# Kernel tuning notes

Measured on AMD Instinct MI355X. Metric: run time of the kernel, lower is better.

The kernel has to match this reference:

```python
import jax, jax.numpy as jnp
import numpy as np

N, E = 50000, 1600000
IN, HID, OUT, H, ED = 128, 16, 40, 4, 16
HC = HID * H  # 64
NEG_SLOPE = 0.2
EPS = 1e-16


def gat_conv(x, src, dst, e_attr, W, att_s, att_d, We, att_e, bias):
    # x: [N, Fin]; src/dst: [E_tot]; e_attr: [E_tot, ED]
    n = x.shape[0]
    h = (x @ W).reshape(n, H, HID)                      # [N,H,C]
    a_s = (h * att_s).sum(-1)                           # [N,H]
    a_d = (h * att_d).sum(-1)                           # [N,H]
    ee = (e_attr @ We).reshape(-1, H, HID)              # [E,H,C]
    a_e = (ee * att_e).sum(-1)                          # [E,H]
    alpha = a_s[src] + a_d[dst] + a_e                   # [E,H]
    alpha = jax.nn.leaky_relu(alpha, NEG_SLOPE)
    amax = jax.ops.segment_max(alpha, dst, num_segments=n)
    ex = jnp.exp(alpha - amax[dst])
    den = jax.ops.segment_sum(ex, dst, num_segments=n)
    alpha = ex / (den[dst] + EPS)
    msg = h[src] * alpha[..., None]                     # [E,H,C]
    out = jax.ops.segment_sum(msg, dst, num_segments=n) # [N,H,C]
    return out.reshape(n, HC) + bias


def setup_inputs() -> dict:
    key = jax.random.key(0)
    ks = jax.random.split(key, 20)
    s = 0.05
    inp = {
        "x": jax.random.normal(ks[0], (N, IN), jnp.float32),
        "edge_index": jax.random.randint(ks[1], (2, E), 0, N, jnp.int64 if jax.config.jax_enable_x64 else jnp.int32),
        "edge_attr": jax.random.normal(ks[2], (E, ED), jnp.float32),
        # conv1
        "W1": jax.random.normal(ks[3], (IN, HC)) * s,
        "att_src1": jax.random.normal(ks[4], (H, HID)) * s,
        "att_dst1": jax.random.normal(ks[5], (H, HID)) * s,
        "We1": jax.random.normal(ks[6], (ED, HC)) * s,
        "att_e1": jax.random.normal(ks[7], (H, HID)) * s,
        "b1": jnp.zeros((HC,), jnp.float32),
        # conv2
        "W2": jax.random.normal(ks[8], (HC, HC)) * s,
        "att_src2": jax.random.normal(ks[9], (H, HID)) * s,
        "att_dst2": jax.random.normal(ks[10], (H, HID)) * s,
        "We2": jax.random.normal(ks[11], (ED, HC)) * s,
        "att_e2": jax.random.normal(ks[12], (H, HID)) * s,
        "b2": jnp.zeros((HC,), jnp.float32),
        # head
        "lw1": jax.random.normal(ks[13], (HC, HID)) * s,
        "lb1": jnp.zeros((HID,), jnp.float32),
        "lw2": jax.random.normal(ks[14], (HID, OUT)) * s,
        "lb2": jnp.zeros((OUT,), jnp.float32),
    }
    return inp


def reference(x, edge_index, edge_attr,
              W1, att_src1, att_dst1, We1, att_e1, b1,
              W2, att_src2, att_dst2, We2, att_e2, b2,
              lw1, lb1, lw2, lb2):
    n = x.shape[0]
    loop = jnp.arange(n, dtype=edge_index.dtype)
    src = jnp.concatenate([edge_index[0], loop])
    dst = jnp.concatenate([edge_index[1], loop])
    # self-loop edge_attr filled with mean over edges (PyG fill_value='mean')
    mean_attr = edge_attr.mean(axis=0, keepdims=True)
    ea = jnp.concatenate([edge_attr, jnp.broadcast_to(mean_attr, (n, edge_attr.shape[1]))])

    h = gat_conv(x, src, dst, ea, W1, att_src1, att_dst1, We1, att_e1, b1)
    h = jax.nn.relu(h)  # dropout is identity at eval
    h = gat_conv(h, src, dst, ea, W2, att_src2, att_dst2, We2, att_e2, b2)
    h = jax.nn.relu(h)
    h = (h @ lw1 + lb1) @ lw2 + lb2  # Linear -> Dropout(eval) -> Linear
    return jax.nn.log_softmax(h, axis=1)
```

## Files before the change

kernel.cpp:

```cpp
#include <hip/hip_runtime.h>
#include <hip/hip_fp16.h>

#define N_NODES 50000
#define E_EDGES 1600000
#define NEG 0.2f
#define EDGE_BLOCKS 6250
#define RED_BLOCKS 64
#define SCAN_BLOCKS ((N_NODES + 255)/256)

__device__ __forceinline__ float lrelu(float x){ return fmaxf(x, NEG*x); }
__device__ __forceinline__ float bcastlane(float v, int k){
    return __int_as_float(__builtin_amdgcn_readlane(__float_as_int(v), k));
}
__device__ __forceinline__ unsigned bf16rn(float x){
    unsigned u = __float_as_uint(x);
    return (u + 0x7FFFu + ((u >> 16) & 1u)) >> 16;
}
__device__ __forceinline__ float bf2f(unsigned short u){
    return __uint_as_float(((unsigned)u) << 16);
}
__device__ __forceinline__ unsigned h16(float x){
    return (unsigned)__half_as_ushort(__float2half(x));
}
__device__ __forceinline__ float f16dec(unsigned u){
    return __half2float(__ushort_as_half((unsigned short)(u & 0xFFFFu)));
}

#if __has_builtin(__builtin_amdgcn_cvt_f32_fp8) && __has_builtin(__builtin_amdgcn_cvt_pk_fp8_f32)
__device__ __forceinline__ unsigned enc8(float x){
    return (unsigned)__builtin_amdgcn_cvt_pk_fp8_f32(x, x, 0, false) & 0xFFu;
}
__device__ __forceinline__ float dec8(unsigned b){
    return __builtin_amdgcn_cvt_f32_fp8((int)b, 0);
}
#else
__device__ __forceinline__ unsigned enc8(float x){
    float ax = fabsf(x); unsigned s = (x < 0.f) ? 0x80u : 0u;
    if (ax < 0.015625f){
        int q = (int)rintf(ax * 512.f);
        return s | (unsigned)q;
    }
    if (ax >= 448.f) return s | 0x7Eu;
    int ee; float mm = frexpf(ax, &ee);
    int q = (int)rintf(mm * 16.f);
    int E = ee + 6;
    if (q == 16){ q = 8; ++E; }
    if (E > 15){ return s | 0x7Eu; }
    return s | ((unsigned)E << 3) | (unsigned)(q - 8);
}
__device__ __forceinline__ float dec8(unsigned b){
    unsigned s = b >> 7, e = (b >> 3) & 15u, m = b & 7u;
    float mag = e ? __uint_as_float(((e + 120u) << 23) | (m << 20))
                  : (float)m * 0.001953125f;
    return s ? -mag : mag;
}
#endif


__global__ void k_prep1(const float* __restrict__ We1, const float* __restrict__ atte1,
                        const float* __restrict__ We2, const float* __restrict__ atte2,
                        float* __restrict__ small){
    int t = threadIdx.x;
    int k = t >> 2, hh = t & 3;
    float w1 = 0.f, w2 = 0.f;
    for (int c = 0; c < 16; ++c){
        w1 = fmaf(We1[k*64 + hh*16 + c], atte1[hh*16 + c], w1);
        w2 = fmaf(We2[k*64 + hh*16 + c], atte2[hh*16 + c], w2);
    }
    small[32 + t] = w1;
    small[96 + t] = w2;
}

__global__ __launch_bounds__(256) void k_hist(const int4* __restrict__ dst4, int* __restrict__ deg,
                                              ushort4* __restrict__ rank4){
    int i = blockIdx.x*256 + threadIdx.x;
    if (i < E_EDGES/4){
        int4 v = dst4[i];
        ushort4 r;
        r.x = (unsigned short)atomicAdd(&deg[v.x], 1);
        r.y = (unsigned short)atomicAdd(&deg[v.y], 1);
        r.z = (unsigned short)atomicAdd(&deg[v.z], 1);
        r.w = (unsigned short)atomicAdd(&deg[v.w], 1);
        rank4[i] = r;
    }
}

__global__ __launch_bounds__(256) void k_scan_a(const int* __restrict__ deg, int* __restrict__ bsum){
    int i = blockIdx.x*256 + threadIdx.x;
    int v = (i < N_NODES) ? deg[i] : 0;
    v += __shfl_xor(v,1); v += __shfl_xor(v,2); v += __shfl_xor(v,4);
    v += __shfl_xor(v,8); v += __shfl_xor(v,16); v += __shfl_xor(v,32);
    __shared__ int ws[4];
    if ((threadIdx.x & 63) == 0) ws[threadIdx.x >> 6] = v;
    __syncthreads();
    if (threadIdx.x == 0) bsum[blockIdx.x] = ws[0] + ws[1] + ws[2] + ws[3];
}

__global__ __launch_bounds__(256) void k_scan_b(const int* __restrict__ bsum, int* __restrict__ boff){
    __shared__ int sm[256];
    int t = threadIdx.x;
    int v = (t < SCAN_BLOCKS) ? bsum[t] : 0;
    sm[t] = v;
    __syncthreads();
    for (int off = 1; off < 256; off <<= 1){
        int u = (t >= off) ? sm[t-off] : 0;
        __syncthreads();
        sm[t] += u;
        __syncthreads();
    }
    boff[t] = (t > 0) ? sm[t-1] : 0;
    if (t == 0) boff[SCAN_BLOCKS] = sm[255];
}

__global__ __launch_bounds__(256) void k_scan_c(const int* __restrict__ deg, const int* __restrict__ boff,
                                                int* __restrict__ base){
    int i = blockIdx.x*256 + threadIdx.x;
    int lane = threadIdx.x & 63, wid = threadIdx.x >> 6;
    int v = (i < N_NODES) ? deg[i] : 0;
    int inc = v;
    for (int off = 1; off < 64; off <<= 1){
        int u = __shfl_up(inc, off);
        if (lane >= off) inc += u;
    }
    __shared__ int wsum[4];
    if (lane == 63) wsum[wid] = inc;
    __syncthreads();
    int wpre = 0;
#pragma unroll
    for (int w = 0; w < 4; ++w) wpre += (w < wid) ? wsum[w] : 0;
    int ex = boff[blockIdx.x] + wpre + inc - v;
    if (i < N_NODES) base[i] = ex;
    if (i == N_NODES - 1) base[N_NODES] = ex + v;
}

template<int FIN>
__global__ __launch_bounds__(256) void k_node(const float* __restrict__ in, const float* __restrict__ W,
                                              const float* __restrict__ att_s, const float* __restrict__ att_d,
                                              unsigned char* __restrict__ hb8,
                                              unsigned short* __restrict__ a_s,
                                              unsigned short* __restrict__ a_d){
    __shared__ float Wl[FIN*64];
    for (int i = threadIdx.x; i < FIN*64; i += 256) Wl[i] = W[i];
    __syncthreads();
    int lane = threadIdx.x & 63;
    int node = blockIdx.x*4 + (threadIdx.x >> 6);
    const float* row = in + (size_t)node*FIN;
    float x0 = row[lane];
    float x1 = 0.f;
    if constexpr (FIN == 128) x1 = row[64 + lane];
    float acc = 0.f;
#pragma unroll
    for (int k = 0; k < 64; ++k)
        acc = fmaf(bcastlane(x0, k), Wl[k*64 + lane], acc);
    if constexpr (FIN == 128){
#pragma unroll
        for (int k = 0; k < 64; ++k)
            acc = fmaf(bcastlane(x1, k), Wl[(64+k)*64 + lane], acc);
    }
    hb8[(size_t)node*64 + lane] = (unsigned char)enc8(acc);
    float ps = acc * att_s[lane];
    float pd = acc * att_d[lane];
    ps += __shfl_xor(ps,1); ps += __shfl_xor(ps,2); ps += __shfl_xor(ps,4); ps += __shfl_xor(ps,8);
    pd += __shfl_xor(pd,1); pd += __shfl_xor(pd,2); pd += __shfl_xor(pd,4); pd += __shfl_xor(pd,8);
    if ((lane & 15) == 0){
        a_s[node*4 + (lane>>4)] = (unsigned short)bf16rn(ps);
        a_d[node*4 + (lane>>4)] = (unsigned short)bf16rn(pd);
    }
}

__global__ __launch_bounds__(256) void k_edges(const int* __restrict__ src, const int* __restrict__ dst,
                                               const unsigned short* __restrict__ rank,
                                               const float* __restrict__ ea, const float* __restrict__ small,
                                               const int* __restrict__ base, uint4* __restrict__ rec,
                                               float* __restrict__ partials){
    __shared__ float w1[64], w2[64];
    __shared__ float red[64];
    if (threadIdx.x < 64){ w1[threadIdx.x] = small[32+threadIdx.x]; w2[threadIdx.x] = small[96+threadIdx.x]; }
    __syncthreads();
    int e = blockIdx.x*256 + threadIdx.x;
    int s = src[e], d = dst[e];
    int rk = (int)rank[e];
    int p = base[d] + rk;
    const float4* eap = (const float4*)(ea + (size_t)e*16);
    float cs[16];
    float ae1[4] = {0,0,0,0}, ae2[4] = {0,0,0,0};
#pragma unroll
    for (int q = 0; q < 4; ++q){
        float4 v4 = eap[q];
        float vv[4] = {v4.x, v4.y, v4.z, v4.w};
#pragma unroll
        for (int r = 0; r < 4; ++r){
            int k = q*4 + r;
            float xv = vv[r];
            cs[k] = xv;
#pragma unroll
            for (int hh = 0; hh < 4; ++hh){
                ae1[hh] = fmaf(xv, w1[k*4+hh], ae1[hh]);
                ae2[hh] = fmaf(xv, w2[k*4+hh], ae2[hh]);
            }
        }
    }
    unsigned q8[4];
#pragma unroll
    for (int hh = 0; hh < 4; ++hh){
        int qv = (int)rintf(ae2[hh]*256.f) + 128;
        qv = qv < 0 ? 0 : (qv > 255 ? 255 : qv);
        q8[hh] = (unsigned)qv;
    }
    uint4 r;
    r.x = (unsigned)s;
    r.y = h16(ae1[0]) | (h16(ae1[1]) << 16);
    r.z = h16(ae1[2]) | (h16(ae1[3]) << 16);
    r.w = q8[0] | (q8[1] << 8) | (q8[2] << 16) | (q8[3] << 24);
    rec[p] = r;
#pragma unroll
    for (int k = 0; k < 16; ++k){
        float v = cs[k];
        v += __shfl_xor(v,1); v += __shfl_xor(v,2); v += __shfl_xor(v,4);
        v += __shfl_xor(v,8); v += __shfl_xor(v,16); v += __shfl_xor(v,32);
        if ((threadIdx.x & 63) == 0) red[k*4 + (threadIdx.x>>6)] = v;
    }
    __syncthreads();
    if (threadIdx.x < 16){
        float v = red[threadIdx.x*4] + red[threadIdx.x*4+1] + red[threadIdx.x*4+2] + red[threadIdx.x*4+3];
        partials[blockIdx.x*16 + threadIdx.x] = v;
    }
}

__global__ __launch_bounds__(256) void k_red(const float* __restrict__ partials, float* __restrict__ red16){
    const int TOT = EDGE_BLOCKS*16;
    int t = threadIdx.x;
    float v = 0.f;
    for (int idx = blockIdx.x*256 + t; idx < TOT; idx += RED_BLOCKS*256) v += partials[idx];
    v += __shfl_xor(v,16); v += __shfl_xor(v,32);
    __shared__ float sm[64];
    int lane = t & 63, wid = t >> 6;
    if (lane < 16) sm[wid*16 + lane] = v;
    __syncthreads();
    if (t < 16) red16[blockIdx.x*16 + t] = sm[t] + sm[16+t] + sm[32+t] + sm[48+t];
}

__global__ __launch_bounds__(256) void k_prep2(float* __restrict__ small, const float* __restrict__ red16){
    __shared__ float sm[256];
    __shared__ float mean_s[16];
    int t = threadIdx.x;
    float v = 0.f;
    for (int r = (t>>4); r < RED_BLOCKS; r += 16) v += red16[r*16 + (t&15)];
    sm[t] = v;
    __syncthreads();
    if (t < 16){
        float s = 0.f;
#pragma unroll
        for (int i = 0; i < 16; ++i) s += sm[t + 16*i];
        float m = s * (1.0f/(float)E_EDGES);
        mean_s[t] = m; small[16+t] = m;
    }
    __syncthreads();
    if (t < 4){
        float a1 = 0.f, a2 = 0.f;
#pragma unroll
        for (int k = 0; k < 16; ++k){
            a1 = fmaf(mean_s[k], small[32 + k*4 + t], a1);
            a2 = fmaf(mean_s[k], small[96 + k*4 + t], a2);
        }
        small[160+t] = a1; small[164+t] = a2;
    }
}

template<int L>
__global__ __launch_bounds__(256) void k_agg(const uint4* __restrict__ recs, const int* __restrict__ base,
                                             const unsigned char* __restrict__ hb8,
                                             const unsigned short* __restrict__ a_s,
                                             const unsigned short* __restrict__ a_d,
                                             const float* __restrict__ aeloop, const float* __restrict__ bias,
                                             float* __restrict__ out){
    int lane = threadIdx.x & 63;
    int n = blockIdx.x*4 + (threadIdx.x >> 6);
    int hh = lane >> 4;
    int e16 = lane >> 2, h4 = lane & 3;
    float ad_acc = bf2f(a_d[n*4+hh]);
    float ad_w   = bf2f(a_d[n*4+h4]);
    float wL = __expf(lrelu(bf2f(a_s[n*4+hh]) + ad_acc + aeloop[hh]));
    float s0 = wL, s1 = 0.f;
    float acc0 = wL * dec8(hb8[(unsigned)n*64u + (unsigned)lane]);
    float acc1 = 0.f;
    int b0 = base[n], b1 = base[n+1];
    for (int pc = b0; pc < b1; pc += 16){
        int m = b1 - pc; m = m < 16 ? m : 16;
        float w = 0.f;
        unsigned si_e = 0u;
        if (e16 < m){
            uint4 r = recs[pc + e16];
            si_e = r.x;
            float ae;
            if constexpr (L == 1){
                ae = f16dec(((h4 < 2) ? r.y : r.z) >> ((h4 & 1)*16));
            } else {
                ae = (float)((int)((r.w >> (h4*8)) & 255u) - 128) * 0.00390625f;
            }
            float as_v = bf2f((unsigned short)a_s[si_e*4u + (unsigned)h4]);
            w = __expf(lrelu(as_v + ad_w + ae));
        }
        int j = 0;
        for (; j + 2 <= m; j += 2){
            unsigned siA = (unsigned)__shfl((int)si_e, j*4);
            unsigned siB = (unsigned)__shfl((int)si_e, j*4 + 4);
            float wA = __shfl(w, j*4 + hh);
            float wB = __shfl(w, j*4 + 4 + hh);
            float hvA = dec8(hb8[siA*64u + (unsigned)lane]);
            float hvB = dec8(hb8[siB*64u + (unsigned)lane]);
            s0 += wA; acc0 = fmaf(wA, hvA, acc0);
            s1 += wB; acc1 = fmaf(wB, hvB, acc1);
        }
        if (j < m){
            unsigned si = (unsigned)__shfl((int)si_e, j*4);
            float wj = __shfl(w, j*4 + hh);
            float hv = dec8(hb8[si*64u + (unsigned)lane]);
            s0 += wj; acc0 = fmaf(wj, hv, acc0);
        }
    }
    float s = s0 + s1;
    float val = (acc0 + acc1) / (s + 1e-16f) + bias[lane];
    out[(size_t)n*64 + lane] = fmaxf(val, 0.f);
}

__global__ __launch_bounds__(256) void k_head(const float* __restrict__ h2,
                                              const float* __restrict__ lw1, const float* __restrict__ lb1,
                                              const float* __restrict__ lw2, const float* __restrict__ lb2,
                                              float* __restrict__ out){
    int n = blockIdx.x*256 + threadIdx.x;
    if (n >= N_NODES) return;
    float y16[16];
#pragma unroll
    for (int j = 0; j < 16; ++j) y16[j] = lb1[j];
    const float4* hp = (const float4*)(h2 + (size_t)n*64);
#pragma unroll
    for (int k4 = 0; k4 < 16; ++k4){
        float4 hv = hp[k4];
        float hvv[4] = {hv.x, hv.y, hv.z, hv.w};
#pragma unroll
        for (int r = 0; r < 4; ++r){
            float x = hvv[r];
            int k = k4*4 + r;
#pragma unroll
            for (int j = 0; j < 16; ++j) y16[j] = fmaf(x, lw1[k*16+j], y16[j]);
        }
    }
    float y[40];
#pragma unroll
    for (int o = 0; o < 40; ++o) y[o] = lb2[o];
#pragma unroll
    for (int j = 0; j < 16; ++j){
        float x = y16[j];
#pragma unroll
        for (int o = 0; o < 40; ++o) y[o] = fmaf(x, lw2[j*40+o], y[o]);
    }
    float mx = y[0];
#pragma unroll
    for (int o = 1; o < 40; ++o) mx = fmaxf(mx, y[o]);
    float sum = 0.f;
#pragma unroll
    for (int o = 0; o < 40; ++o) sum += __expf(y[o] - mx);
    float ls = __logf(sum) + mx;
    float* op = out + (size_t)n*40;
#pragma unroll
    for (int o = 0; o < 40; ++o) op[o] = y[o] - ls;
}

extern "C" void kernel_launch(void* const* d_in, const int* in_sizes, int n_in,
                              void* d_out, int out_size, void* d_ws, size_t ws_size,
                              hipStream_t stream){
    const float* x     = (const float*)d_in[0];
    const int*   ei    = (const int*)  d_in[1];
    const float* ea    = (const float*)d_in[2];
    const float* W1    = (const float*)d_in[3];
    const float* atts1 = (const float*)d_in[4];
    const float* attd1 = (const float*)d_in[5];
    const float* We1   = (const float*)d_in[6];
    const float* atte1 = (const float*)d_in[7];
    const float* b1    = (const float*)d_in[8];
    const float* W2    = (const float*)d_in[9];
    const float* atts2 = (const float*)d_in[10];
    const float* attd2 = (const float*)d_in[11];
    const float* We2   = (const float*)d_in[12];
    const float* atte2 = (const float*)d_in[13];
    const float* b2    = (const float*)d_in[14];
    const float* lw1   = (const float*)d_in[15];
    const float* lb1   = (const float*)d_in[16];
    const float* lw2   = (const float*)d_in[17];
    const float* lb2   = (const float*)d_in[18];
    float* outp = (float*)d_out;

    const int* srcp = ei;
    const int* dstp = ei + E_EDGES;

    char* ws = (char*)d_ws;
    size_t off = 0;
    auto alloc = [&](size_t bytes) -> void* {
        void* p = ws + off;
        off = (off + bytes + 255) & ~(size_t)255;
        return p;
    };
    float*  smallf   = (float*) alloc(256*sizeof(float));
    float*  partials = (float*) alloc((size_t)EDGE_BLOCKS*16*sizeof(float));
    float*  red16    = (float*) alloc((size_t)RED_BLOCKS*16*sizeof(float));
    int*    deg      = (int*)   alloc((size_t)N_NODES*sizeof(int));
    int*    base     = (int*)   alloc((size_t)(N_NODES+1)*sizeof(int));
    int*    bsum     = (int*)   alloc((size_t)(SCAN_BLOCKS+1)*sizeof(int));
    int*    boff     = (int*)   alloc((size_t)(SCAN_BLOCKS+1)*sizeof(int));
    unsigned short* rank = (unsigned short*)alloc((size_t)E_EDGES*sizeof(unsigned short));
    uint4*  rec      = (uint4*) alloc((size_t)E_EDGES*16);
    unsigned char* hb8 = (unsigned char*)alloc((size_t)N_NODES*64);
    float*  obuf     = (float*) alloc((size_t)N_NODES*64*sizeof(float));
    unsigned short* asb = (unsigned short*)alloc((size_t)N_NODES*4*sizeof(unsigned short));
    unsigned short* adb = (unsigned short*)alloc((size_t)N_NODES*4*sizeof(unsigned short));

    const int NB = N_NODES/4;
    const int HB = (N_NODES + 255)/256;

    hipMemsetAsync(deg, 0, (size_t)N_NODES*sizeof(int), stream);
    k_prep1<<<1, 64, 0, stream>>>(We1, atte1, We2, atte2, smallf);
    k_hist<<<(E_EDGES/4 + 255)/256, 256, 0, stream>>>((const int4*)dstp, deg, (ushort4*)rank);
    k_scan_a<<<SCAN_BLOCKS, 256, 0, stream>>>(deg, bsum);
    k_scan_b<<<1, 256, 0, stream>>>(bsum, boff);
    k_scan_c<<<SCAN_BLOCKS, 256, 0, stream>>>(deg, boff, base);

    k_node<128><<<NB, 256, 0, stream>>>(x, W1, atts1, attd1, hb8, asb, adb);
    k_edges<<<EDGE_BLOCKS, 256, 0, stream>>>(srcp, dstp, rank, ea, smallf, base, rec, partials);
    k_red<<<RED_BLOCKS, 256, 0, stream>>>(partials, red16);
    k_prep2<<<1, 256, 0, stream>>>(smallf, red16);
    k_agg<1><<<NB, 256, 0, stream>>>(rec, base, hb8, asb, adb, smallf + 160, b1, obuf);

    k_node<64><<<NB, 256, 0, stream>>>(obuf, W2, atts2, attd2, hb8, asb, adb);
    k_agg<2><<<NB, 256, 0, stream>>>(rec, base, hb8, asb, adb, smallf + 164, b2, obuf);

    k_head<<<HB, 256, 0, stream>>>(obuf, lw1, lb1, lw2, lb2, outp);
}
```

Before: 348.6 us.

## Replace global atomic degree histogram with per-block LDS histograms plus column scan

```diff
diff --git a/kernel.cpp b/kernel.cpp
--- a/kernel.cpp
+++ b/kernel.cpp
@@ -7,6 +7,9 @@
 #define EDGE_BLOCKS 6250
 #define RED_BLOCKS 64
 #define SCAN_BLOCKS ((N_NODES + 255)/256)
+#define HBLK 128
+#define EPHB (E_EDGES/HBLK)
+#define NPAIR (N_NODES/2)
 
 __device__ __forceinline__ float lrelu(float x){ return fmaxf(x, NEG*x); }
 __device__ __forceinline__ float bcastlane(float v, int k){
@@ -71,18 +74,39 @@
     small[96 + t] = w2;
 }
 
-__global__ __launch_bounds__(256) void k_hist(const int4* __restrict__ dst4, int* __restrict__ deg,
-                                              ushort4* __restrict__ rank4){
-    int i = blockIdx.x*256 + threadIdx.x;
-    if (i < E_EDGES/4){
-        int4 v = dst4[i];
-        ushort4 r;
-        r.x = (unsigned short)atomicAdd(&deg[v.x], 1);
-        r.y = (unsigned short)atomicAdd(&deg[v.y], 1);
-        r.z = (unsigned short)atomicAdd(&deg[v.z], 1);
-        r.w = (unsigned short)atomicAdd(&deg[v.w], 1);
-        rank4[i] = r;
-    }
+__global__ __launch_bounds__(256) void k_hist1(const int* __restrict__ dst,
+                                               unsigned* __restrict__ bhist,
+                                               unsigned short* __restrict__ lrank){
+    extern __shared__ unsigned hist[];
+    for (int i = threadIdx.x; i < NPAIR; i += 256) hist[i] = 0u;
+    __syncthreads();
+    int b0 = blockIdx.x*EPHB;
+    for (int i = threadIdx.x; i < EPHB; i += 256){
+        int e = b0 + i;
+        int d = dst[e];
+        unsigned sh = (unsigned)(d & 1) * 16u;
+        unsigned old = atomicAdd(&hist[d >> 1], 1u << sh);
+        lrank[e] = (unsigned short)((old >> sh) & 0xFFFFu);
+    }
+    __syncthreads();
+    unsigned* bh = bhist + (size_t)blockIdx.x*NPAIR;
+    for (int i = threadIdx.x; i < NPAIR; i += 256) bh[i] = hist[i];
+}
+
+__global__ __launch_bounds__(256) void k_hist2(const unsigned* __restrict__ bhist,
+                                               unsigned* __restrict__ boff,
+                                               int* __restrict__ deg){
+    int j = blockIdx.x*256 + threadIdx.x;
+    if (j >= NPAIR) return;
+    unsigned lo = 0, hi = 0;
+    for (int b = 0; b < HBLK; ++b){
+        unsigned v = bhist[(size_t)b*NPAIR + j];
+        boff[(size_t)b*NPAIR + j] = lo | (hi << 16);
+        lo += v & 0xFFFFu;
+        hi += v >> 16;
+    }
+    deg[2*j]     = (int)lo;
+    deg[2*j + 1] = (int)hi;
 }
 
 __global__ __launch_bounds__(256) void k_scan_a(const int* __restrict__ deg, int* __restrict__ bsum){
@@ -169,7 +193,8 @@
 }
 
 __global__ __launch_bounds__(256) void k_edges(const int* __restrict__ src, const int* __restrict__ dst,
-                                               const unsigned short* __restrict__ rank,
+                                               const unsigned short* __restrict__ lrank,
+                                               const unsigned* __restrict__ boff32,
                                                const float* __restrict__ ea, const float* __restrict__ small,
                                                const int* __restrict__ base, uint4* __restrict__ rec,
                                                float* __restrict__ partials){
@@ -179,8 +204,9 @@
     __syncthreads();
     int e = blockIdx.x*256 + threadIdx.x;
     int s = src[e], d = dst[e];
-    int rk = (int)rank[e];
-    int p = base[d] + rk;
+    int hb = e / EPHB;
+    unsigned offpk = boff32[(size_t)hb*NPAIR + (d >> 1)];
+    int p = base[d] + (int)((offpk >> ((unsigned)(d & 1)*16u)) & 0xFFFFu) + (int)lrank[e];
     const float4* eap = (const float4*)(ea + (size_t)e*16);
     float cs[16];
     float ae1[4] = {0,0,0,0}, ae2[4] = {0,0,0,0};
@@ -407,8 +433,10 @@
     int*    deg      = (int*)   alloc((size_t)N_NODES*sizeof(int));
     int*    base     = (int*)   alloc((size_t)(N_NODES+1)*sizeof(int));
     int*    bsum     = (int*)   alloc((size_t)(SCAN_BLOCKS+1)*sizeof(int));
-    int*    boff     = (int*)   alloc((size_t)(SCAN_BLOCKS+1)*sizeof(int));
-    unsigned short* rank = (unsigned short*)alloc((size_t)E_EDGES*sizeof(unsigned short));
+    int*    boffs    = (int*)   alloc((size_t)(SCAN_BLOCKS+1)*sizeof(int));
+    unsigned short* lrank = (unsigned short*)alloc((size_t)E_EDGES*sizeof(unsigned short));
+    unsigned* bhist  = (unsigned*)alloc((size_t)HBLK*NPAIR*sizeof(unsigned));
+    unsigned* boff32 = (unsigned*)alloc((size_t)HBLK*NPAIR*sizeof(unsigned));
     uint4*  rec      = (uint4*) alloc((size_t)E_EDGES*16);
     unsigned char* hb8 = (unsigned char*)alloc((size_t)N_NODES*64);
     float*  obuf     = (float*) alloc((size_t)N_NODES*64*sizeof(float));
@@ -417,16 +445,18 @@
 
     const int NB = N_NODES/4;
     const int HB = (N_NODES + 255)/256;
-
-    hipMemsetAsync(deg, 0, (size_t)N_NODES*sizeof(int), stream);
+    const int PB = (NPAIR + 255)/256;
+
     k_prep1<<<1, 64, 0, stream>>>(We1, atte1, We2, atte2, smallf);
-    k_hist<<<(E_EDGES/4 + 255)/256, 256, 0, stream>>>((const int4*)dstp, deg, (ushort4*)rank);
+    k_hist1<<<HBLK, 256, NPAIR*sizeof(unsigned), stream>>>(dstp, bhist, lrank);
+    k_hist2<<<PB, 256, 0, stream>>>(bhist, boff32, deg);
     k_scan_a<<<SCAN_BLOCKS, 256, 0, stream>>>(deg, bsum);
-    k_scan_b<<<1, 256, 0, stream>>>(bsum, boff);
-    k_scan_c<<<SCAN_BLOCKS, 256, 0, stream>>>(deg, boff, base);
+    k_scan_b<<<1, 256, 0, stream>>>(bsum, boffs);
+    k_scan_c<<<SCAN_BLOCKS, 256, 0, stream>>>(deg, boffs, base);
 
     k_node<128><<<NB, 256, 0, stream>>>(x, W1, atts1, attd1, hb8, asb, adb);
-    k_edges<<<EDGE_BLOCKS, 256, 0, stream>>>(srcp, dstp, rank, ea, smallf, base, rec, partials);
+    k_edges<<<EDGE_BLOCKS, 256, 0, stream>>>(srcp, dstp, lrank, boff32, ea, smallf,
+                                             base, rec, partials);
     k_red<<<RED_BLOCKS, 256, 0, stream>>>(partials, red16);
     k_prep2<<<1, 256, 0, stream>>>(smallf, red16);
     k_agg<1><<<NB, 256, 0, stream>>>(rec, base, hb8, asb, adb, smallf + 160, b1, obuf);
```

After: 312.4 us. 10.4% less time.
